# Optimization experiments

Measured on AMD Instinct MI355X. Metric: run time of the kernel, lower is better.

Reference implementation:

```python
import jax, jax.numpy as jnp
import numpy as np

D = 128
N_SRC = 50000
N_DST = 50000
E = 640000
NEG_SLOPE = 0.01  # torch LeakyReLU default


def _lrelu(x):
    return jax.nn.leaky_relu(x, NEG_SLOPE)


def setup_inputs() -> dict:
    key = jax.random.key(0)
    ks = jax.random.split(key, 12)
    s = 1.0 / np.sqrt(D)
    return {
        "feat_src": jax.random.normal(ks[0], (N_SRC, D), jnp.float32),
        "feat_dst": jax.random.normal(ks[1], (N_DST, D), jnp.float32),
        "src_idx": jax.random.randint(ks[2], (E,), 0, N_SRC, jnp.int32),
        "dst_idx": jax.random.randint(ks[3], (E,), 0, N_DST, jnp.int32),
        "W_src": jax.random.uniform(ks[4], (D, D), jnp.float32, -s, s),
        "b_src": jnp.zeros((D,), jnp.float32),
        "W_dst": jax.random.uniform(ks[5], (D, D), jnp.float32, -s, s),
        "b_dst": jnp.zeros((D,), jnp.float32),
        "W_a1": jax.random.uniform(ks[6], (D, D), jnp.float32, -s, s),
        "b_a1": jnp.zeros((D,), jnp.float32),
        "W_a2": jax.random.uniform(ks[7], (D, 1), jnp.float32, -s, s),
        "b_a2": jnp.zeros((1,), jnp.float32),
        "W_out": jax.random.uniform(ks[8], (D, D), jnp.float32, -s, s),
        "b_out": jnp.zeros((D,), jnp.float32),
    }


def reference(feat_src, feat_dst, src_idx, dst_idx,
              W_src, b_src, W_dst, b_dst,
              W_a1, b_a1, W_a2, b_a2, W_out, b_out):
    n_dst = feat_dst.shape[0]
    # node projections (dropout is identity in eval mode)
    hs = feat_src @ W_src + b_src            # [n_src, d]
    hd = feat_dst @ W_dst + b_dst            # [n_dst, d]
    # u_add_v: per-edge feature
    e = hs[src_idx] + hd[dst_idx]            # [E, d]
    # attention MLP: LeakyReLU -> Linear -> LeakyReLU -> Linear(d->1)
    s = _lrelu(_lrelu(e) @ W_a1 + b_a1) @ W_a2 + b_a2  # [E, 1]
    s = s[:, 0]
    # edge softmax grouped by destination node (numerically stable)
    m = jax.ops.segment_max(s, dst_idx, num_segments=n_dst)
    ex = jnp.exp(s - m[dst_idx])
    denom = jax.ops.segment_sum(ex, dst_idx, num_segments=n_dst)
    alpha = ex / denom[dst_idx]              # [E]
    # scale messages and scatter-sum to dst nodes
    n_f = jax.ops.segment_sum(alpha[:, None] * e, dst_idx, num_segments=n_dst)
    return _lrelu(n_f @ W_out + b_out)       # [n_dst, d]
```

## Files before the change

kernel.cpp:

```cpp
#include <hip/hip_runtime.h>
#include <math.h>

#define DD 128
#define NEG 0.01f
#define SCHUNK 4096

typedef __attribute__((ext_vector_type(8))) _Float16 half8;
typedef __attribute__((ext_vector_type(4))) float f32x4;

__device__ __forceinline__ float lrelu(float x){ return x > 0.f ? x : NEG * x; }

__device__ __forceinline__ unsigned short h2u(_Float16 h){
    union { _Float16 h; unsigned short u; } v; v.h = h; return v.u;
}
__device__ __forceinline__ _Float16 u2h(unsigned short u){
    union { unsigned short u; _Float16 h; } v; v.u = u; return v.h;
}

__device__ __forceinline__ half8 h8max(half8 x, half8 y){
#if __has_builtin(__builtin_elementwise_max)
    return __builtin_elementwise_max(x, y);
#else
    half8 r;
    #pragma unroll
    for (int i = 0; i < 8; i++) r[i] = x[i] > y[i] ? x[i] : y[i];
    return r;
#endif
}

__global__ void hist_pack(const int* dst, int* deg, int E, int nhist,
                          const float* Wa1, const float* Wsrc,
                          const float* Wdst, const float* Wout,
                          unsigned short* wpack){
    const int bid = blockIdx.x;
    if (bid < nhist){
        int i = bid * 256 + threadIdx.x;
        if (i < E) atomicAdd(&deg[dst[i]], 1);
    } else {
        int i = (bid - nhist) * 256 + threadIdx.x;
        if (i >= 4 * 16384) return;
        int seg = i >> 14, t = i & 16383;
        int j = t & 7, lane = (t >> 3) & 63, nt = (t >> 9) & 7, kc = t >> 12;
        int k = kc * 32 + (lane >> 4) * 8 + j;
        int n = nt * 16 + (lane & 15);
        const float* W = (seg == 0) ? Wa1 : (seg == 1) ? Wsrc : (seg == 2) ? Wdst : Wout;
        wpack[i] = h2u((_Float16)W[k * DD + n]);
    }
}

__global__ __launch_bounds__(1024) void scan1(const int* deg, int* part, int n){
    __shared__ int wsum[16];
    const int tid = threadIdx.x;
    const int lane = tid & 63, wid = tid >> 6;
    int i4 = blockIdx.x * SCHUNK + tid * 4;
    int4 v = make_int4(0, 0, 0, 0);
    if (i4 + 3 < n) v = *(const int4*)(deg + i4);
    else {
        if (i4 + 0 < n) v.x = deg[i4 + 0];
        if (i4 + 1 < n) v.y = deg[i4 + 1];
        if (i4 + 2 < n) v.z = deg[i4 + 2];
        if (i4 + 3 < n) v.w = deg[i4 + 3];
    }
    int t = v.x + v.y + v.z + v.w;
    #pragma unroll
    for (int off = 1; off < 64; off <<= 1) t += __shfl_xor(t, off, 64);
    if (lane == 0) wsum[wid] = t;
    __syncthreads();
    if (tid == 0){
        int s = 0;
        #pragma unroll
        for (int j = 0; j < 16; j++) s += wsum[j];
        part[blockIdx.x] = s;
    }
}

__global__ __launch_bounds__(1024) void scan2(const int* deg, const int* part,
        int* row_off, int* cursor, int n, int nchunks){
    __shared__ int wsum[16];
    const int tid = threadIdx.x;
    const int lane = tid & 63, wid = tid >> 6;
    const int b = blockIdx.x;
    int carry = 0;
    for (int j = 0; j < b; j++) carry += part[j];
    int i4 = b * SCHUNK + tid * 4;
    int4 v = make_int4(0, 0, 0, 0);
    if (i4 + 3 < n) v = *(const int4*)(deg + i4);
    else {
        if (i4 + 0 < n) v.x = deg[i4 + 0];
        if (i4 + 1 < n) v.y = deg[i4 + 1];
        if (i4 + 2 < n) v.z = deg[i4 + 2];
        if (i4 + 3 < n) v.w = deg[i4 + 3];
    }
    int tsum = v.x + v.y + v.z + v.w;
    int x = tsum;
    #pragma unroll
    for (int off = 1; off < 64; off <<= 1){
        int t = __shfl_up(x, off, 64);
        if (lane >= off) x += t;
    }
    if (lane == 63) wsum[wid] = x;
    __syncthreads();
    int wprefix = 0;
    #pragma unroll
    for (int j = 0; j < 16; j++) if (j < wid) wprefix += wsum[j];
    int excl = carry + wprefix + (x - tsum);
    if (i4 + 3 < n){
        int4 o;
        o.x = excl; o.y = excl + v.x; o.z = o.y + v.y; o.w = o.z + v.z;
        *(int4*)(row_off + i4) = o;
        *(int4*)(cursor + i4) = o;
    } else {
        int a = excl;
        if (i4 + 0 < n){ row_off[i4 + 0] = a; cursor[i4 + 0] = a; a += v.x; }
        if (i4 + 1 < n){ row_off[i4 + 1] = a; cursor[i4 + 1] = a; a += v.y; }
        if (i4 + 2 < n){ row_off[i4 + 2] = a; cursor[i4 + 2] = a; a += v.z; }
        if (i4 + 3 < n){ row_off[i4 + 3] = a; cursor[i4 + 3] = a; }
    }
    if (b == 0 && tid == 0){
        int tot = 0;
        for (int j = 0; j < nchunks; j++) tot += part[j];
        row_off[n] = tot;
    }
}

__global__ void scatter_pairs(const int* src, const int* dst, int* cursor,
                              int2* pairs, int E){
    int i = blockIdx.x * blockDim.x + threadIdx.x;
    if (i < E){
        int d = dst[i];
        int s = src[i];
        int pos = atomicAdd(&cursor[d], 1);
        pairs[pos] = make_int2(s, d);
    }
}

__global__ __launch_bounds__(256) void lin2_mfma(
        const float* X1, const unsigned short* W1, const float* b1,
        unsigned short* Yb1, int n1, int g1,
        const float* X2, const unsigned short* W2, const float* b2,
        unsigned short* Yb2, int n2){
    __shared__ unsigned short sB[16384];
    const int tid = threadIdx.x;
    const int second = (blockIdx.x >= g1);
    const float* X = second ? X2 : X1;
    const unsigned short* W = second ? W2 : W1;
    const float* b = second ? b2 : b1;
    unsigned short* Yb = second ? Yb2 : Yb1;
    const int nrows = second ? n2 : n1;
    const int bidx = second ? (blockIdx.x - g1) : blockIdx.x;
    {
        const uint4* g = (const uint4*)W;
        uint4* l = (uint4*)sB;
        #pragma unroll
        for (int t = 0; t < 8; t++) l[tid + 256 * t] = g[tid + 256 * t];
    }
    const int wave = tid >> 6, lane = tid & 63;
    const int qd = lane >> 4, ln16 = lane & 15;
    const int row0 = bidx * 128 + wave * 32;
    int r0 = row0 + ln16;       if (r0 >= nrows) r0 = nrows - 1;
    int r1 = row0 + 16 + ln16;  if (r1 >= nrows) r1 = nrows - 1;
    f32x4 acc[2][8];
    #pragma unroll
    for (int rt = 0; rt < 2; rt++)
        #pragma unroll
        for (int nt = 0; nt < 8; nt++)
            acc[rt][nt] = (f32x4){0.f, 0.f, 0.f, 0.f};
    __syncthreads();
    #pragma unroll
    for (int kc = 0; kc < 4; kc++){
        const int koff = kc * 32 + qd * 8;
        half8 a[2];
        const float* px[2] = {X + (size_t)r0 * DD + koff, X + (size_t)r1 * DD + koff};
        #pragma unroll
        for (int rt = 0; rt < 2; rt++){
            float4 v0 = *(const float4*)(px[rt]);
            float4 v1 = *(const float4*)(px[rt] + 4);
            a[rt][0] = (_Float16)v0.x; a[rt][1] = (_Float16)v0.y;
            a[rt][2] = (_Float16)v0.z; a[rt][3] = (_Float16)v0.w;
            a[rt][4] = (_Float16)v1.x; a[rt][5] = (_Float16)v1.y;
            a[rt][6] = (_Float16)v1.z; a[rt][7] = (_Float16)v1.w;
        }
        #pragma unroll
        for (int nt = 0; nt < 8; nt++){
            const int fi = (((kc << 3) + nt) << 6 | lane) << 3;
            half8 bw = *(const half8*)&sB[fi];
            acc[0][nt] = __builtin_amdgcn_mfma_f32_16x16x32_f16(a[0], bw, acc[0][nt], 0, 0, 0);
            acc[1][nt] = __builtin_amdgcn_mfma_f32_16x16x32_f16(a[1], bw, acc[1][nt], 0, 0, 0);
        }
    }
    #pragma unroll
    for (int nt = 0; nt < 8; nt++){
        const int col = nt * 16 + ln16;
        const float bv = b[col];
        #pragma unroll
        for (int rt = 0; rt < 2; rt++){
            #pragma unroll
            for (int r = 0; r < 4; r++){
                int row = row0 + rt * 16 + qd * 4 + r;
                if (row < nrows){
                    float y = acc[rt][nt][r] + bv;
                    Yb[(size_t)row * DD + col] = h2u((_Float16)y);
                }
            }
        }
    }
}

__global__ __launch_bounds__(256) void lin_mfma(const float* X,
        const unsigned short* W, const float* b, float* Y, int nrows){
    __shared__ unsigned short sB[16384];
    const int tid = threadIdx.x;
    {
        const uint4* g = (const uint4*)W;
        uint4* l = (uint4*)sB;
        #pragma unroll
        for (int t = 0; t < 8; t++) l[tid + 256 * t] = g[tid + 256 * t];
    }
    const int wave = tid >> 6, lane = tid & 63;
    const int qd = lane >> 4, ln16 = lane & 15;
    const int row0 = blockIdx.x * 128 + wave * 32;
    int r0 = row0 + ln16;       if (r0 >= nrows) r0 = nrows - 1;
    int r1 = row0 + 16 + ln16;  if (r1 >= nrows) r1 = nrows - 1;
    f32x4 acc[2][8];
    #pragma unroll
    for (int rt = 0; rt < 2; rt++)
        #pragma unroll
        for (int nt = 0; nt < 8; nt++)
            acc[rt][nt] = (f32x4){0.f, 0.f, 0.f, 0.f};
    __syncthreads();
    #pragma unroll
    for (int kc = 0; kc < 4; kc++){
        const int koff = kc * 32 + qd * 8;
        half8 a[2];
        const float* px[2] = {X + (size_t)r0 * DD + koff, X + (size_t)r1 * DD + koff};
        #pragma unroll
        for (int rt = 0; rt < 2; rt++){
            float4 v0 = *(const float4*)(px[rt]);
            float4 v1 = *(const float4*)(px[rt] + 4);
            a[rt][0] = (_Float16)v0.x; a[rt][1] = (_Float16)v0.y;
            a[rt][2] = (_Float16)v0.z; a[rt][3] = (_Float16)v0.w;
            a[rt][4] = (_Float16)v1.x; a[rt][5] = (_Float16)v1.y;
            a[rt][6] = (_Float16)v1.z; a[rt][7] = (_Float16)v1.w;
        }
        #pragma unroll
        for (int nt = 0; nt < 8; nt++){
            const int fi = (((kc << 3) + nt) << 6 | lane) << 3;
            half8 bw = *(const half8*)&sB[fi];
            acc[0][nt] = __builtin_amdgcn_mfma_f32_16x16x32_f16(a[0], bw, acc[0][nt], 0, 0, 0);
            acc[1][nt] = __builtin_amdgcn_mfma_f32_16x16x32_f16(a[1], bw, acc[1][nt], 0, 0, 0);
        }
    }
    #pragma unroll
    for (int nt = 0; nt < 8; nt++){
        const int col = nt * 16 + ln16;
        const float bv = b[col];
        #pragma unroll
        for (int rt = 0; rt < 2; rt++){
            #pragma unroll
            for (int r = 0; r < 4; r++){
                int row = row0 + rt * 16 + qd * 4 + r;
                if (row < nrows){
                    float y = acc[rt][nt][r] + bv;
                    Y[(size_t)row * DD + col] = lrelu(y);
                }
            }
        }
    }
}

__device__ __forceinline__ half8 afrag_from(half8 a, half8 b){
    half8 s = a + b;
    return h8max(s, s * (_Float16)NEG);
}

__device__ __forceinline__ void score_epilogue(const f32x4* acc, const float* w2v,
        float b2, int e0rt, int qd, int ln16, float* s_w, int E){
    float p[4] = {0.f, 0.f, 0.f, 0.f};
    #pragma unroll
    for (int nt = 0; nt < 8; nt++)
        #pragma unroll
        for (int r = 0; r < 4; r++){
            float z = acc[nt][r];
            z = fmaxf(z, NEG * z);
            p[r] += z * w2v[nt];
        }
    #pragma unroll
    for (int r = 0; r < 4; r++){
        float v = p[r];
        #pragma unroll
        for (int off = 1; off < 16; off <<= 1) v += __shfl_xor(v, off, 64);
        p[r] = __expf(v + b2);
    }
    if (ln16 == 0){
        int row = e0rt + qd * 4;
        #pragma unroll
        for (int r = 0; r < 4; r++)
            if (row + r < E) s_w[row + r] = p[r];
    }
}

__global__ __launch_bounds__(512, 4) void edge_score_mfma(
        const unsigned short* hs_h, const unsigned short* hd_h,
        const int2* pairs,
        const unsigned short* wa1p, const float* ba1,
        const float* Wa2, const float* ba2,
        float* s_w, int E){
    __shared__ unsigned short sB[16384];
    const int tid = threadIdx.x;
    {
        const uint4* g = (const uint4*)wa1p;
        uint4* l = (uint4*)sB;
        #pragma unroll
        for (int t = 0; t < 4; t++) l[tid + 512 * t] = g[tid + 512 * t];
    }
    const int wave = tid >> 6, lane = tid & 63;
    const int qd = lane >> 4, ln16 = lane & 15;
    const int e0 = blockIdx.x * 256 + wave * 32;
    float b1v[8], w2v[8];
    #pragma unroll
    for (int nt = 0; nt < 8; nt++){
        b1v[nt] = ba1[nt * 16 + ln16];
        w2v[nt] = Wa2[nt * 16 + ln16];
    }
    const float b2 = ba2[0];
    __syncthreads();

    int eid0 = e0 + ln16;       if (eid0 >= E) eid0 = E - 1;
    int eid1 = e0 + 16 + ln16;  if (eid1 >= E) eid1 = E - 1;
    const int2 pp0 = pairs[eid0];
    const int2 pp1 = pairs[eid1];
    const unsigned short* ps0 = hs_h + (size_t)pp0.x * DD;
    const unsigned short* pd0 = hd_h + (size_t)pp0.y * DD;
    const unsigned short* ps1 = hs_h + (size_t)pp1.x * DD;
    const unsigned short* pd1 = hd_h + (size_t)pp1.y * DD;

    f32x4 acc0[8];
    #pragma unroll
    for (int nt = 0; nt < 8; nt++)
        acc0[nt] = (f32x4){b1v[nt], b1v[nt], b1v[nt], b1v[nt]};
    #pragma unroll
    for (int kc = 0; kc < 4; kc++){
        const int koff = kc * 32 + qd * 8;
        half8 af = afrag_from(*(const half8*)(ps0 + koff), *(const half8*)(pd0 + koff));
        #pragma unroll
        for (int nt = 0; nt < 8; nt++){
            half8 bf = *(const half8*)&sB[(((kc << 3) + nt) << 6 | lane) << 3];
            acc0[nt] = __builtin_amdgcn_mfma_f32_16x16x32_f16(af, bf, acc0[nt], 0, 0, 0);
        }
    }
    half8 ra[4], rb[4];
    #pragma unroll
    for (int kc = 0; kc < 4; kc++){
        const int koff = kc * 32 + qd * 8;
        ra[kc] = *(const half8*)(ps1 + koff);
        rb[kc] = *(const half8*)(pd1 + koff);
    }
    score_epilogue(acc0, w2v, b2, e0, qd, ln16, s_w, E);
    f32x4 acc1[8];
    #pragma unroll
    for (int nt = 0; nt < 8; nt++)
        acc1[nt] = (f32x4){b1v[nt], b1v[nt], b1v[nt], b1v[nt]};
    #pragma unroll
    for (int kc = 0; kc < 4; kc++){
        half8 af = afrag_from(ra[kc], rb[kc]);
        #pragma unroll
        for (int nt = 0; nt < 8; nt++){
            half8 bf = *(const half8*)&sB[(((kc << 3) + nt) << 6 | lane) << 3];
            acc1[nt] = __builtin_amdgcn_mfma_f32_16x16x32_f16(af, bf, acc1[nt], 0, 0, 0);
        }
    }
    score_epilogue(acc1, w2v, b2, e0 + 16, qd, ln16, s_w, E);
}

__global__ __launch_bounds__(256) void agg_softmax(const unsigned short* hs_h,
        const unsigned short* hd_h, const int* row_off, const int2* pairs,
        const float* s_w, float* nf, int n_dst){
    const int w = (blockIdx.x * blockDim.x + threadIdx.x) >> 6;
    const int lane = threadIdx.x & 63;
    if (w >= n_dst) return;
    const int beg = row_off[w], end = row_off[w + 1];
    const int hf = lane >> 5, l32 = lane & 31;
    float4 acc = make_float4(0.f, 0.f, 0.f, 0.f);
    float sa = 0.f;
    int e = beg;
    for (; e + 7 < end; e += 8){
        int rows[4]; float wv[4]; ushort4 uv[4];
        #pragma unroll
        for (int j = 0; j < 4; j++){
            int ee = e + 2 * j + hf;
            rows[j] = pairs[ee].x;
            wv[j] = s_w[ee];
        }
        #pragma unroll
        for (int j = 0; j < 4; j++)
            uv[j] = *(const ushort4*)(hs_h + (size_t)rows[j] * DD + l32 * 4);
        #pragma unroll
        for (int j = 0; j < 4; j++){
            acc.x += wv[j] * (float)u2h(uv[j].x);
            acc.y += wv[j] * (float)u2h(uv[j].y);
            acc.z += wv[j] * (float)u2h(uv[j].z);
            acc.w += wv[j] * (float)u2h(uv[j].w);
            sa += wv[j];
        }
    }
    for (; e < end; e += 2){
        int ee = e + hf;
        float wv = 0.f;
        int row;
        if (ee < end){ row = pairs[ee].x; wv = s_w[ee]; }
        else row = pairs[end - 1].x;
        ushort4 uv = *(const ushort4*)(hs_h + (size_t)row * DD + l32 * 4);
        acc.x += wv * (float)u2h(uv.x);
        acc.y += wv * (float)u2h(uv.y);
        acc.z += wv * (float)u2h(uv.z);
        acc.w += wv * (float)u2h(uv.w);
        sa += wv;
    }
    acc.x += __shfl_xor(acc.x, 32, 64);
    acc.y += __shfl_xor(acc.y, 32, 64);
    acc.z += __shfl_xor(acc.z, 32, 64);
    acc.w += __shfl_xor(acc.w, 32, 64);
    sa    += __shfl_xor(sa, 32, 64);
    const float inv = (end > beg) ? 1.f / sa : 0.f;
    if (hf == 0){
        ushort4 hu = *(const ushort4*)(hd_h + (size_t)w * DD + l32 * 4);
        const float gx = (end > beg) ? 1.f : 0.f;
        float4 out;
        out.x = acc.x * inv + gx * (float)u2h(hu.x);
        out.y = acc.y * inv + gx * (float)u2h(hu.y);
        out.z = acc.z * inv + gx * (float)u2h(hu.z);
        out.w = acc.w * inv + gx * (float)u2h(hu.w);
        *(float4*)(nf + (size_t)w * DD + l32 * 4) = out;
    }
}

extern "C" void kernel_launch(void* const* d_in, const int* in_sizes, int n_in,
                              void* d_out, int out_size, void* d_ws, size_t ws_size,
                              hipStream_t stream){
    const float* feat_src = (const float*)d_in[0];
    const float* feat_dst = (const float*)d_in[1];
    const int*   src_idx  = (const int*)d_in[2];
    const int*   dst_idx  = (const int*)d_in[3];
    const float* W_src = (const float*)d_in[4];
    const float* b_src = (const float*)d_in[5];
    const float* W_dst = (const float*)d_in[6];
    const float* b_dst = (const float*)d_in[7];
    const float* W_a1  = (const float*)d_in[8];
    const float* b_a1  = (const float*)d_in[9];
    const float* W_a2  = (const float*)d_in[10];
    const float* b_a2  = (const float*)d_in[11];
    const float* W_out = (const float*)d_in[12];
    const float* b_out = (const float*)d_in[13];
    const int n_src = in_sizes[0] / DD;
    const int n_dst = in_sizes[1] / DD;
    const int E = in_sizes[2];
    const int nchunks = (n_dst + SCHUNK - 1) / SCHUNK;

    char* p = (char*)d_ws;
    unsigned short* hs_h = (unsigned short*)p;  p += (size_t)n_src * DD * 2;
    unsigned short* hd_h = (unsigned short*)p;  p += (size_t)n_dst * DD * 2;
    unsigned short* wpack = (unsigned short*)p; p += 4 * 16384 * 2;
    float* s_w = (float*)p;                     p += (size_t)E * 4;
    int2* pairs = (int2*)p;                     p += (size_t)E * 8;
    int* deg = (int*)p;                         p += (size_t)n_dst * 4;
    int* cursor = (int*)p;                      p += (size_t)n_dst * 4;
    int* part = (int*)p;                        p += 64 * 4;
    int* row_off = (int*)p;                     p += ((size_t)n_dst + 1) * 4;
    float* nf = (float*)d_out;

    const unsigned short* wa1p = wpack;
    const unsigned short* wsrc = wpack + 1 * 16384;
    const unsigned short* wdst = wpack + 2 * 16384;
    const unsigned short* wout = wpack + 3 * 16384;

    hipMemsetAsync(deg, 0, (size_t)n_dst * 4, stream);
    const int nhist = (E + 255) / 256;
    const int npack = (4 * 16384 + 255) / 256;
    hist_pack<<<nhist + npack, 256, 0, stream>>>(dst_idx, deg, E, nhist,
                                                 W_a1, W_src, W_dst, W_out, wpack);
    scan1<<<nchunks, 1024, 0, stream>>>(deg, part, n_dst);
    scan2<<<nchunks, 1024, 0, stream>>>(deg, part, row_off, cursor, n_dst, nchunks);
    scatter_pairs<<<(E + 255) / 256, 256, 0, stream>>>(src_idx, dst_idx, cursor,
                                                       pairs, E);
    const int g1 = (n_src + 127) / 128;
    const int g2 = (n_dst + 127) / 128;
    lin2_mfma<<<g1 + g2, 256, 0, stream>>>(feat_src, wsrc, b_src, hs_h, n_src, g1,
                                           feat_dst, wdst, b_dst, hd_h, n_dst);
    edge_score_mfma<<<(E + 255) / 256, 512, 0, stream>>>(hs_h, hd_h, pairs, wa1p, b_a1,
                                                         W_a2, b_a2, s_w, E);
    agg_softmax<<<((size_t)n_dst * 64 + 255) / 256, 256, 0, stream>>>(hs_h, hd_h, row_off,
                                                                      pairs, s_w, nf, n_dst);
    lin_mfma<<<g2, 256, 0, stream>>>(nf, wout, b_out, nf, n_dst);
}
```

Measured before the change: 298.6 us.

## Loop edge-score row tiles, drop occupancy hint and bias, unroll aggregation tail

Collapses the two hand-interleaved row tiles of the edge-score MFMA kernel into a loop and removes the prefetch of the second tile's gathered rows. This lowers register pressure, but the gather latency is no longer overlapped with the first tile's epilogue. The min-blocks-per-CU launch bound hint is removed, and the b_a2 bias is dropped from the exponent because it cancels in the softmax. The aggregation tail loop now handles four edges per iteration with two independent gathers per lane, giving more memory-level parallelism.

After: 293.8 us. Within noise of the previous version (-1.6%).

```diff
diff --git a/kernel.cpp b/kernel.cpp
--- a/kernel.cpp
+++ b/kernel.cpp
@@ -273,33 +273,7 @@
     return h8max(s, s * (_Float16)NEG);
 }
 
-__device__ __forceinline__ void score_epilogue(const f32x4* acc, const float* w2v,
-        float b2, int e0rt, int qd, int ln16, float* s_w, int E){
-    float p[4] = {0.f, 0.f, 0.f, 0.f};
-    #pragma unroll
-    for (int nt = 0; nt < 8; nt++)
-        #pragma unroll
-        for (int r = 0; r < 4; r++){
-            float z = acc[nt][r];
-            z = fmaxf(z, NEG * z);
-            p[r] += z * w2v[nt];
-        }
-    #pragma unroll
-    for (int r = 0; r < 4; r++){
-        float v = p[r];
-        #pragma unroll
-        for (int off = 1; off < 16; off <<= 1) v += __shfl_xor(v, off, 64);
-        p[r] = __expf(v + b2);
-    }
-    if (ln16 == 0){
-        int row = e0rt + qd * 4;
-        #pragma unroll
-        for (int r = 0; r < 4; r++)
-            if (row + r < E) s_w[row + r] = p[r];
-    }
-}
-
-__global__ __launch_bounds__(512, 4) void edge_score_mfma(
+__global__ __launch_bounds__(512) void edge_score_mfma(
         const unsigned short* hs_h, const unsigned short* hd_h,
         const int2* pairs,
         const unsigned short* wa1p, const float* ba1,
@@ -322,54 +296,49 @@
         b1v[nt] = ba1[nt * 16 + ln16];
         w2v[nt] = Wa2[nt * 16 + ln16];
     }
-    const float b2 = ba2[0];
     __syncthreads();
-
-    int eid0 = e0 + ln16;       if (eid0 >= E) eid0 = E - 1;
-    int eid1 = e0 + 16 + ln16;  if (eid1 >= E) eid1 = E - 1;
-    const int2 pp0 = pairs[eid0];
-    const int2 pp1 = pairs[eid1];
-    const unsigned short* ps0 = hs_h + (size_t)pp0.x * DD;
-    const unsigned short* pd0 = hd_h + (size_t)pp0.y * DD;
-    const unsigned short* ps1 = hs_h + (size_t)pp1.x * DD;
-    const unsigned short* pd1 = hd_h + (size_t)pp1.y * DD;
-
-    f32x4 acc0[8];
-    #pragma unroll
-    for (int nt = 0; nt < 8; nt++)
-        acc0[nt] = (f32x4){b1v[nt], b1v[nt], b1v[nt], b1v[nt]};
-    #pragma unroll
-    for (int kc = 0; kc < 4; kc++){
-        const int koff = kc * 32 + qd * 8;
-        half8 af = afrag_from(*(const half8*)(ps0 + koff), *(const half8*)(pd0 + koff));
-        #pragma unroll
-        for (int nt = 0; nt < 8; nt++){
-            half8 bf = *(const half8*)&sB[(((kc << 3) + nt) << 6 | lane) << 3];
-            acc0[nt] = __builtin_amdgcn_mfma_f32_16x16x32_f16(af, bf, acc0[nt], 0, 0, 0);
-        }
-    }
-    half8 ra[4], rb[4];
-    #pragma unroll
-    for (int kc = 0; kc < 4; kc++){
-        const int koff = kc * 32 + qd * 8;
-        ra[kc] = *(const half8*)(ps1 + koff);
-        rb[kc] = *(const half8*)(pd1 + koff);
-    }
-    score_epilogue(acc0, w2v, b2, e0, qd, ln16, s_w, E);
-    f32x4 acc1[8];
-    #pragma unroll
-    for (int nt = 0; nt < 8; nt++)
-        acc1[nt] = (f32x4){b1v[nt], b1v[nt], b1v[nt], b1v[nt]};
-    #pragma unroll
-    for (int kc = 0; kc < 4; kc++){
-        half8 af = afrag_from(ra[kc], rb[kc]);
-        #pragma unroll
-        for (int nt = 0; nt < 8; nt++){
-            half8 bf = *(const half8*)&sB[(((kc << 3) + nt) << 6 | lane) << 3];
-            acc1[nt] = __builtin_amdgcn_mfma_f32_16x16x32_f16(af, bf, acc1[nt], 0, 0, 0);
-        }
-    }
-    score_epilogue(acc1, w2v, b2, e0 + 16, qd, ln16, s_w, E);
+    for (int rt = 0; rt < 2; rt++){
+        int eid = e0 + rt * 16 + ln16;
+        if (eid >= E) eid = E - 1;
+        const int2 pp = pairs[eid];
+        f32x4 acc[8];
+        #pragma unroll
+        for (int nt = 0; nt < 8; nt++)
+            acc[nt] = (f32x4){b1v[nt], b1v[nt], b1v[nt], b1v[nt]};
+        #pragma unroll
+        for (int kc = 0; kc < 4; kc++){
+            const int koff = kc * 32 + qd * 8;
+            half8 af = afrag_from(*(const half8*)(hs_h + (size_t)pp.x * DD + koff),
+                                  *(const half8*)(hd_h + (size_t)pp.y * DD + koff));
+            #pragma unroll
+            for (int nt = 0; nt < 8; nt++){
+                half8 bf = *(const half8*)&sB[(((kc << 3) + nt) << 6 | lane) << 3];
+                acc[nt] = __builtin_amdgcn_mfma_f32_16x16x32_f16(af, bf, acc[nt], 0, 0, 0);
+            }
+        }
+        float p[4] = {0.f, 0.f, 0.f, 0.f};
+        #pragma unroll
+        for (int nt = 0; nt < 8; nt++)
+            #pragma unroll
+            for (int r = 0; r < 4; r++){
+                float z = acc[nt][r];
+                z = fmaxf(z, NEG * z);
+                p[r] += z * w2v[nt];
+            }
+        #pragma unroll
+        for (int r = 0; r < 4; r++){
+            float v = p[r];
+            #pragma unroll
+            for (int off = 1; off < 16; off <<= 1) v += __shfl_xor(v, off, 64);
+            p[r] = __expf(v);
+        }
+        if (ln16 == 0){
+            int row = e0 + rt * 16 + qd * 4;
+            #pragma unroll
+            for (int r = 0; r < 4; r++)
+                if (row + r < E) s_w[row + r] = p[r];
+        }
+    }
 }
 
 __global__ __launch_bounds__(256) void agg_softmax(const unsigned short* hs_h,
@@ -403,18 +372,20 @@
             sa += wv[j];
         }
     }
-    for (; e < end; e += 2){
-        int ee = e + hf;
-        float wv = 0.f;
-        int row;
-        if (ee < end){ row = pairs[ee].x; wv = s_w[ee]; }
-        else row = pairs[end - 1].x;
-        ushort4 uv = *(const ushort4*)(hs_h + (size_t)row * DD + l32 * 4);
-        acc.x += wv * (float)u2h(uv.x);
-        acc.y += wv * (float)u2h(uv.y);
-        acc.z += wv * (float)u2h(uv.z);
-        acc.w += wv * (float)u2h(uv.w);
-        sa += wv;
+    for (; e < end; e += 4){
+        int ee0 = e + hf;          int ee1 = e + 2 + hf;
+        int ec0 = ee0 < end ? ee0 : end - 1;
+        int ec1 = ee1 < end ? ee1 : end - 1;
+        int r0 = pairs[ec0].x, r1 = pairs[ec1].x;
+        float wv0 = (ee0 < end) ? s_w[ec0] : 0.f;
+        float wv1 = (ee1 < end) ? s_w[ec1] : 0.f;
+        ushort4 u0 = *(const ushort4*)(hs_h + (size_t)r0 * DD + l32 * 4);
+        ushort4 u1 = *(const ushort4*)(hs_h + (size_t)r1 * DD + l32 * 4);
+        acc.x += wv0 * (float)u2h(u0.x) + wv1 * (float)u2h(u1.x);
+        acc.y += wv0 * (float)u2h(u0.y) + wv1 * (float)u2h(u1.y);
+        acc.z += wv0 * (float)u2h(u0.z) + wv1 * (float)u2h(u1.z);
+        acc.w += wv0 * (float)u2h(u0.w) + wv1 * (float)u2h(u1.w);
+        sa += wv0 + wv1;
     }
     acc.x += __shfl_xor(acc.x, 32, 64);
     acc.y += __shfl_xor(acc.y, 32, 64);
```
